# Kernel tuning notes

Measured on AMD Instinct MI355X. Metric: run time of the kernel, lower is better.

The kernel has to match this reference:

```python
import jax, jax.numpy as jnp
import numpy as np

NEG_SLOPE = 0.2


def _gat_layer(x, W, a_src, a_dst, b, src, dst, n_nodes, heads, dim):
    # x: [N, F_in]; W: [F_in, heads*dim]
    h = (x @ W).reshape(n_nodes, heads, dim)            # [N,H,D]
    e_src = (h * a_src).sum(-1)                          # [N,H]
    e_dst = (h * a_dst).sum(-1)                          # [N,H]
    e = jax.nn.leaky_relu(e_src[src] + e_dst[dst], NEG_SLOPE)  # [E,H]
    # edge softmax over incoming edges of each target node
    m = jax.ops.segment_max(e, dst, num_segments=n_nodes)      # [N,H]
    ex = jnp.exp(e - m[dst])
    denom = jax.ops.segment_sum(ex, dst, num_segments=n_nodes)  # [N,H]
    alpha = ex / denom[dst]                              # [E,H]
    out = jax.ops.segment_sum(h[src] * alpha[:, :, None], dst,
                              num_segments=n_nodes)      # [N,H,D]
    return out.reshape(n_nodes, heads * dim) + b


def setup_inputs() -> dict:
    key = jax.random.key(0)
    ks = jax.random.split(key, 10)
    N, E, F_in = 100000, 1600000, 300
    x = jax.random.normal(ks[0], (N, F_in), dtype=jnp.float32)
    edge_index = jax.random.randint(ks[1], (2, E), 0, N, dtype=jnp.int64)
    s = 0.1
    return {
        'x': x,
        'edge_index': edge_index,
        'W1': jax.random.normal(ks[2], (F_in, 64), jnp.float32) * s,
        'att_src1': jax.random.normal(ks[3], (8, 8), jnp.float32) * s,
        'att_dst1': jax.random.normal(ks[4], (8, 8), jnp.float32) * s,
        'b1': jax.random.normal(ks[5], (64,), jnp.float32) * s,
        'W2': jax.random.normal(ks[6], (64, 64), jnp.float32) * s,
        'att_src2': jax.random.normal(ks[7], (1, 64), jnp.float32) * s,
        'att_dst2': jax.random.normal(ks[8], (1, 64), jnp.float32) * s,
        'b2': jax.random.normal(ks[9], (64,), jnp.float32) * s,
    }


def reference(x, edge_index, W1, att_src1, att_dst1, b1, W2, att_src2, att_dst2, b2):
    N = x.shape[0]
    # add self-loops (PyG GATConv default)
    loop = jnp.arange(N, dtype=edge_index.dtype)
    src = jnp.concatenate([edge_index[0], loop])
    dst = jnp.concatenate([edge_index[1], loop])
    # dropout p=0.6 is identity in eval mode
    h = _gat_layer(x, W1, att_src1, att_dst1, b1, src, dst, N, 8, 8)    # [N,64]
    h = jax.nn.elu(h)
    h = _gat_layer(h, W2, att_src2, att_dst2, b2, src, dst, N, 1, 64)   # [N,64]
    return jax.nn.log_softmax(h, axis=1)
```

## Files before the change

### kernel.cpp

```cpp
#include <hip/hip_runtime.h>
#include <math.h>

using short8  = __attribute__((ext_vector_type(8))) short;
using ushort8 = __attribute__((ext_vector_type(8))) unsigned short;
using f32x4   = __attribute__((ext_vector_type(4))) float;

#define NBLKS 512
#define BPAD  800
#define EB 4

__device__ __forceinline__ unsigned short f2bf(float f) {
    unsigned u = __float_as_uint(f);
    unsigned r = u + 0x7FFF + ((u >> 16) & 1);
    return (unsigned short)(r >> 16);
}
__device__ __forceinline__ float bf2f(unsigned short v) {
    return __uint_as_float((unsigned)v << 16);
}
__device__ __forceinline__ unsigned cvt2(float lo, float hi) {
    unsigned r;
    asm("v_cvt_pk_bf16_f32 %0, %1, %2" : "=v"(r) : "v"(lo), "v"(hi));
    return r;
}


__global__ void detect64_kernel(const int* __restrict__ ei, int E, int* __restrict__ flag) {
    __shared__ int any;
    if (threadIdx.x == 0) any = 0;
    __syncthreads();
    for (int i = threadIdx.x; i < 1024; i += 256) {
        if (ei[2 * i + 1] != 0) { any = 1; break; }
    }
    __syncthreads();
    if (threadIdx.x == 0) *flag = (any ? 0 : 1);
}


__global__ __launch_bounds__(256) void binA_kernel(
    const int* __restrict__ ei, int E, int N, const int* __restrict__ flag,
    int nbuck, int* __restrict__ hist, int chunk) {
    __shared__ int lh[BPAD];
    for (int i = threadIdx.x; i < nbuck; i += 256) lh[i] = 0;
    __syncthreads();
    int is64 = *flag;
    int Etot = E + N;
    int beg = blockIdx.x * chunk, end = min(Etot, beg + chunk);
    for (int i = beg + threadIdx.x; i < end; i += 256) {
        int d = (i < E) ? (is64 ? ei[2 * (E + i)] : ei[E + i]) : (i - E);
        atomicAdd(&lh[d >> 7], 1);
    }
    __syncthreads();
    for (int i = threadIdx.x; i < nbuck; i += 256) hist[blockIdx.x * BPAD + i] = lh[i];
}

__global__ void scanBlocks_kernel(int* __restrict__ hist, int nbuck, int* __restrict__ bucketTotal) {
    int bin = blockIdx.x * 256 + threadIdx.x;
    if (bin >= nbuck) return;
    int run = 0;
    for (int b = 0; b < NBLKS; b++) {
        int v = hist[b * BPAD + bin];
        hist[b * BPAD + bin] = run;
        run += v;
    }
    bucketTotal[bin] = run;
}

__global__ void scanBucket_kernel(const int* __restrict__ bucketTotal, int nbuck,
                                  int* __restrict__ bucketBase) {
    __shared__ int s[1024];
    int t = threadIdx.x;
    int v = (t < nbuck) ? bucketTotal[t] : 0;
    s[t] = v;
    __syncthreads();
    for (int off = 1; off < 1024; off <<= 1) {
        int x = (t >= off) ? s[t - off] : 0;
        __syncthreads();
        s[t] += x;
        __syncthreads();
    }
    if (t < nbuck) bucketBase[t] = s[t] - v;
    if (t == nbuck - 1) bucketBase[nbuck] = s[t];
}

__global__ __launch_bounds__(256) void binB_kernel(
    const int* __restrict__ ei, int E, int N, const int* __restrict__ flag,
    int nbuck, const int* __restrict__ hist, const int* __restrict__ bucketBase,
    int* __restrict__ tmp, int chunk) {
    __shared__ int cur[BPAD];
    for (int i = threadIdx.x; i < nbuck; i += 256)
        cur[i] = bucketBase[i] + hist[blockIdx.x * BPAD + i];
    __syncthreads();
    int is64 = *flag;
    int Etot = E + N;
    int beg = blockIdx.x * chunk, end = min(Etot, beg + chunk);
    for (int i = beg + threadIdx.x; i < end; i += 256) {
        int s, d;
        if (i < E) {
            if (is64) { s = ei[2 * i]; d = ei[2 * (E + i)]; }
            else      { s = ei[i];     d = ei[E + i]; }
        } else { s = i - E; d = i - E; }
        int pos = atomicAdd(&cur[d >> 7], 1);
        tmp[pos] = ((d & 127) << 17) | s;
    }
}

__global__ __launch_bounds__(256) void binC_kernel(
    const int* __restrict__ tmp, const int* __restrict__ bucketBase, int nbuck,
    int N, int Etot, int* __restrict__ rowptr, int* __restrict__ col) {
    __shared__ int lh[128];
    __shared__ int cur[128];
    int g = blockIdx.x;
    int t = threadIdx.x;
    int beg = bucketBase[g], end = bucketBase[g + 1];
    if (t < 128) lh[t] = 0;
    __syncthreads();
    for (int i = beg + t; i < end; i += 256) atomicAdd(&lh[tmp[i] >> 17], 1);
    __syncthreads();
    int c = (t < 128) ? lh[t] : 0;
    for (int off = 1; off < 128; off <<= 1) {
        int x = 0;
        if (t < 128 && t >= off) x = lh[t - off];
        __syncthreads();
        if (t < 128) lh[t] += x;
        __syncthreads();
    }
    if (t < 128) {
        int excl = lh[t] - c;
        cur[t] = beg + excl;
        int node = g * 128 + t;
        if (node < N) rowptr[node] = beg + excl;
    }
    if (g == 0 && t == 0) rowptr[N] = Etot;
    if (g == 0 && t < 16) col[Etot + t] = 0;
    __syncthreads();
    for (int i = beg + t; i < end; i += 256) {
        int v = tmp[i];
        int pos = atomicAdd(&cur[v >> 17], 1);
        col[pos] = v & 0x1FFFF;
    }
}


__global__ __launch_bounds__(256) void gemm1_mfma_kernel(
    const float* __restrict__ x, const float* __restrict__ W,
    const float* __restrict__ asrc, const float* __restrict__ adst,
    unsigned short* __restrict__ hbf, float* __restrict__ es, float* __restrict__ ed, int N) {
    __shared__ __align__(16) unsigned short A_lds[128 * 40];
    __shared__ __align__(16) unsigned short B_lds[64 * 40];
    const int tx = threadIdx.x;
    const int wv = tx >> 6;
    const int lane = tx & 63;
    const int l15 = lane & 15;
    const int quad = lane >> 4;
    const int rowBase = blockIdx.x * 128;

    f32x4 acc[2][4];
#pragma unroll
    for (int rt = 0; rt < 2; rt++)
#pragma unroll
        for (int ct = 0; ct < 4; ct++) acc[rt][ct] = (f32x4){0.f, 0.f, 0.f, 0.f};

    const int kq = tx & 7;
    const int r0 = tx >> 3;
    const int colB = tx & 63;
    const int kkb = (tx >> 6) * 8;

    for (int k0 = 0; k0 < 320; k0 += 32) {
        bool kvalid = (k0 + kq * 4 + 4 <= 300);
#pragma unroll
        for (int p = 0; p < 4; p++) {
            int row = p * 32 + r0;
            int grow = rowBase + row;
            float4 v = make_float4(0.f, 0.f, 0.f, 0.f);
            if (kvalid && grow < N) v = *(const float4*)&x[(size_t)grow * 300 + k0 + kq * 4];
            *(uint2*)&A_lds[row * 40 + kq * 4] = make_uint2(cvt2(v.x, v.y), cvt2(v.z, v.w));
        }
        {
            float v0, v1, v2, v3, v4, v5, v6, v7;
            v0 = (k0 + kkb + 0 < 300) ? W[(size_t)(k0 + kkb + 0) * 64 + colB] : 0.f;
            v1 = (k0 + kkb + 1 < 300) ? W[(size_t)(k0 + kkb + 1) * 64 + colB] : 0.f;
            v2 = (k0 + kkb + 2 < 300) ? W[(size_t)(k0 + kkb + 2) * 64 + colB] : 0.f;
            v3 = (k0 + kkb + 3 < 300) ? W[(size_t)(k0 + kkb + 3) * 64 + colB] : 0.f;
            v4 = (k0 + kkb + 4 < 300) ? W[(size_t)(k0 + kkb + 4) * 64 + colB] : 0.f;
            v5 = (k0 + kkb + 5 < 300) ? W[(size_t)(k0 + kkb + 5) * 64 + colB] : 0.f;
            v6 = (k0 + kkb + 6 < 300) ? W[(size_t)(k0 + kkb + 6) * 64 + colB] : 0.f;
            v7 = (k0 + kkb + 7 < 300) ? W[(size_t)(k0 + kkb + 7) * 64 + colB] : 0.f;
            *(uint2*)&B_lds[colB * 40 + kkb]     = make_uint2(cvt2(v0, v1), cvt2(v2, v3));
            *(uint2*)&B_lds[colB * 40 + kkb + 4] = make_uint2(cvt2(v4, v5), cvt2(v6, v7));
        }
        __syncthreads();
        short8 af[2], bfr[4];
#pragma unroll
        for (int rt = 0; rt < 2; rt++)
            af[rt] = *(const short8*)&A_lds[(wv * 32 + rt * 16 + l15) * 40 + quad * 8];
#pragma unroll
        for (int ct = 0; ct < 4; ct++)
            bfr[ct] = *(const short8*)&B_lds[(ct * 16 + l15) * 40 + quad * 8];
#pragma unroll
        for (int rt = 0; rt < 2; rt++)
#pragma unroll
            for (int ct = 0; ct < 4; ct++)
                acc[rt][ct] = __builtin_amdgcn_mfma_f32_16x16x32_bf16(af[rt], bfr[ct], acc[rt][ct], 0, 0, 0);
        __syncthreads();
    }

    float as_v[4], ad_v[4];
#pragma unroll
    for (int ct = 0; ct < 4; ct++) {
        as_v[ct] = asrc[ct * 16 + l15];
        ad_v[ct] = adst[ct * 16 + l15];
    }
#pragma unroll
    for (int rt = 0; rt < 2; rt++) {
#pragma unroll
        for (int reg = 0; reg < 4; reg++) {
            int row = rowBase + wv * 32 + rt * 16 + quad * 4 + reg;
            bool ok = (row < N);
#pragma unroll
            for (int ct = 0; ct < 4; ct++) {
                float v = acc[rt][ct][reg];
                if (ok) hbf[(size_t)row * 64 + ct * 16 + l15] = f2bf(v);
                float ps = v * as_v[ct];
                float pd = v * ad_v[ct];
                ps += __shfl_xor(ps, 1); ps += __shfl_xor(ps, 2); ps += __shfl_xor(ps, 4);
                pd += __shfl_xor(pd, 1); pd += __shfl_xor(pd, 2); pd += __shfl_xor(pd, 4);
                if ((lane & 7) == 0 && ok) {
                    int head = 2 * ct + ((lane >> 3) & 1);
                    es[row * 8 + head] = ps;
                    ed[row * 8 + head] = pd;
                }
            }
        }
    }
}


__global__ __launch_bounds__(256) void gemm2_mfma_kernel(
    const unsigned short* __restrict__ xin, const float* __restrict__ W,
    const float* __restrict__ asrc, const float* __restrict__ adst,
    unsigned short* __restrict__ hbf, float* __restrict__ es, float* __restrict__ ed, int N) {
    __shared__ __align__(16) unsigned short A_lds[128 * 72];
    __shared__ __align__(16) unsigned short B_lds[64 * 72];
    const int tx = threadIdx.x;
    const int wv = tx >> 6;
    const int lane = tx & 63;
    const int l15 = lane & 15;
    const int quad = lane >> 4;
    const int rowBase = blockIdx.x * 128;

    f32x4 acc[2][4];
#pragma unroll
    for (int rt = 0; rt < 2; rt++)
#pragma unroll
        for (int ct = 0; ct < 4; ct++) acc[rt][ct] = (f32x4){0.f, 0.f, 0.f, 0.f};

    {
        int colB = tx & 63;
        int kk = (tx >> 6) * 16;
#pragma unroll
        for (int j = 0; j < 16; j++)
            B_lds[colB * 72 + kk + j] = f2bf(W[(size_t)(kk + j) * 64 + colB]);
    }
    {
        int kq = tx & 7, r0 = tx >> 3;
        const ushort8 z = (ushort8){0, 0, 0, 0, 0, 0, 0, 0};
#pragma unroll
        for (int p = 0; p < 4; p++) {
            int row = p * 32 + r0;
            int grow = rowBase + row;
            ushort8 v = z;
            if (grow < N) v = *(const ushort8*)&xin[(size_t)grow * 64 + kq * 8];
            *(ushort8*)&A_lds[row * 72 + kq * 8] = v;
        }
    }
    __syncthreads();
#pragma unroll
    for (int c = 0; c < 2; c++) {
        short8 af[2], bfr[4];
#pragma unroll
        for (int rt = 0; rt < 2; rt++)
            af[rt] = *(const short8*)&A_lds[(wv * 32 + rt * 16 + l15) * 72 + quad * 8 + c * 32];
#pragma unroll
        for (int ct = 0; ct < 4; ct++)
            bfr[ct] = *(const short8*)&B_lds[(ct * 16 + l15) * 72 + quad * 8 + c * 32];
#pragma unroll
        for (int rt = 0; rt < 2; rt++)
#pragma unroll
            for (int ct = 0; ct < 4; ct++)
                acc[rt][ct] = __builtin_amdgcn_mfma_f32_16x16x32_bf16(af[rt], bfr[ct], acc[rt][ct], 0, 0, 0);
    }

    float as_v[4], ad_v[4];
#pragma unroll
    for (int ct = 0; ct < 4; ct++) {
        as_v[ct] = asrc[ct * 16 + l15];
        ad_v[ct] = adst[ct * 16 + l15];
    }
#pragma unroll
    for (int rt = 0; rt < 2; rt++) {
#pragma unroll
        for (int reg = 0; reg < 4; reg++) {
            int row = rowBase + wv * 32 + rt * 16 + quad * 4 + reg;
            bool ok = (row < N);
            float ps = 0.f, pd = 0.f;
#pragma unroll
            for (int ct = 0; ct < 4; ct++) {
                float v = acc[rt][ct][reg];
                if (ok) hbf[(size_t)row * 64 + ct * 16 + l15] = f2bf(v);
                ps = fmaf(v, as_v[ct], ps);
                pd = fmaf(v, ad_v[ct], pd);
            }
            ps += __shfl_xor(ps, 1); ps += __shfl_xor(ps, 2);
            ps += __shfl_xor(ps, 4); ps += __shfl_xor(ps, 8);
            pd += __shfl_xor(pd, 1); pd += __shfl_xor(pd, 2);
            pd += __shfl_xor(pd, 4); pd += __shfl_xor(pd, 8);
            if (l15 == 0 && ok) { es[row] = ps; ed[row] = pd; }
        }
    }
}


__global__ __launch_bounds__(256) void agg1f_kernel(
    const int* __restrict__ rowptr, const int* __restrict__ col,
    const unsigned short* __restrict__ hbf, const float* __restrict__ es,
    const float* __restrict__ ed, const float* __restrict__ b,
    unsigned int* __restrict__ outbf, int N) {
    int node = blockIdx.x * 4 + (threadIdx.x >> 6);
    int lane = threadIdx.x & 63;
    if (node >= N) return;
    int half = lane >> 5, fl = lane & 31;
    int f0 = fl * 2, hh = fl >> 2;
    int beg = rowptr[node], end = rowptr[node + 1];
    float edv = ed[node * 8 + hh];
    float acc0 = 0.f, acc1 = 0.f, lsum = 0.f;
    for (int i = beg; i < end; i += 8) {
        int ei_[EB], ss[EB];
        float ev[EB];
        unsigned hp[EB];
#pragma unroll
        for (int j = 0; j < EB; j++) ei_[j] = i + 2 * j + half;
#pragma unroll
        for (int j = 0; j < EB; j++) ss[j] = col[(ei_[j] < end) ? ei_[j] : beg];
#pragma unroll
        for (int j = 0; j < EB; j++) ev[j] = es[ss[j] * 8 + hh];
#pragma unroll
        for (int j = 0; j < EB; j++) hp[j] = *(const unsigned*)&hbf[(size_t)ss[j] * 64 + f0];
#pragma unroll
        for (int j = 0; j < EB; j++) {
            float e = ev[j] + edv;
            e = (e > 0.f) ? e : 0.2f * e;
            float wj = __expf(fminf(e, 30.f));
            wj = (ei_[j] < end) ? wj : 0.f;
            lsum += wj;
            float lo = __uint_as_float(hp[j] << 16);
            float hi = __uint_as_float(hp[j] & 0xFFFF0000u);
            acc0 = fmaf(wj, lo, acc0);
            acc1 = fmaf(wj, hi, acc1);
        }
    }
    acc0 += __shfl_xor(acc0, 32);
    acc1 += __shfl_xor(acc1, 32);
    lsum += __shfl_xor(lsum, 32);
    float rinv = 1.f / lsum;
    float o0 = acc0 * rinv + b[f0];
    float o1 = acc1 * rinv + b[f0 + 1];
    o0 = (o0 > 0.f) ? o0 : expm1f(o0);
    o1 = (o1 > 0.f) ? o1 : expm1f(o1);
    if (half == 0) {
        unsigned pk = (unsigned)f2bf(o0) | ((unsigned)f2bf(o1) << 16);
        outbf[((size_t)node * 64 + f0) >> 1] = pk;
    }
}

__global__ __launch_bounds__(256) void agg2f_kernel(
    const int* __restrict__ rowptr, const int* __restrict__ col,
    const unsigned short* __restrict__ hbf, const float* __restrict__ es,
    const float* __restrict__ ed, const float* __restrict__ b,
    float* __restrict__ out, int N) {
    int node = blockIdx.x * 4 + (threadIdx.x >> 6);
    int lane = threadIdx.x & 63;
    if (node >= N) return;
    int half = lane >> 5, fl = lane & 31;
    int f0 = fl * 2;
    int beg = rowptr[node], end = rowptr[node + 1];
    float edv = ed[node];
    float acc0 = 0.f, acc1 = 0.f, lsum = 0.f;
    for (int i = beg; i < end; i += 8) {
        int ei_[EB], ss[EB];
        float ev[EB];
        unsigned hp[EB];
#pragma unroll
        for (int j = 0; j < EB; j++) ei_[j] = i + 2 * j + half;
#pragma unroll
        for (int j = 0; j < EB; j++) ss[j] = col[(ei_[j] < end) ? ei_[j] : beg];
#pragma unroll
        for (int j = 0; j < EB; j++) ev[j] = es[ss[j]];
#pragma unroll
        for (int j = 0; j < EB; j++) hp[j] = *(const unsigned*)&hbf[(size_t)ss[j] * 64 + f0];
#pragma unroll
        for (int j = 0; j < EB; j++) {
            float e = ev[j] + edv;
            e = (e > 0.f) ? e : 0.2f * e;
            float wj = __expf(fminf(e, 30.f));
            wj = (ei_[j] < end) ? wj : 0.f;
            lsum += wj;
            float lo = __uint_as_float(hp[j] << 16);
            float hi = __uint_as_float(hp[j] & 0xFFFF0000u);
            acc0 = fmaf(wj, lo, acc0);
            acc1 = fmaf(wj, hi, acc1);
        }
    }
    acc0 += __shfl_xor(acc0, 32);
    acc1 += __shfl_xor(acc1, 32);
    lsum += __shfl_xor(lsum, 32);
    float rinv = 1.f / lsum;
    float o0 = acc0 * rinv + b[f0];
    float o1 = acc1 * rinv + b[f0 + 1];
    float M = fmaxf(o0, o1);
    M = fmaxf(M, __shfl_xor(M, 1));  M = fmaxf(M, __shfl_xor(M, 2));
    M = fmaxf(M, __shfl_xor(M, 4));  M = fmaxf(M, __shfl_xor(M, 8));
    M = fmaxf(M, __shfl_xor(M, 16));
    float se = __expf(o0 - M) + __expf(o1 - M);
    se += __shfl_xor(se, 1);  se += __shfl_xor(se, 2);
    se += __shfl_xor(se, 4);  se += __shfl_xor(se, 8);
    se += __shfl_xor(se, 16);
    float ls = logf(se);
    if (half == 0) {
        float2 r = make_float2(o0 - M - ls, o1 - M - ls);
        *(float2*)&out[(size_t)node * 64 + f0] = r;
    }
}


extern "C" void kernel_launch(void* const* d_in, const int* in_sizes, int n_in,
                              void* d_out, int out_size, void* d_ws, size_t ws_size,
                              hipStream_t stream) {
    const float* x   = (const float*)d_in[0];
    const int*   ei  = (const int*)d_in[1];
    const float* W1  = (const float*)d_in[2];
    const float* as1 = (const float*)d_in[3];
    const float* ad1 = (const float*)d_in[4];
    const float* b1  = (const float*)d_in[5];
    const float* W2  = (const float*)d_in[6];
    const float* as2 = (const float*)d_in[7];
    const float* ad2 = (const float*)d_in[8];
    const float* b2  = (const float*)d_in[9];
    const int N = in_sizes[0] / 300;
    const int E = in_sizes[1] / 2;
    const int Etot = E + N;
    const int nbuck = (N + 127) >> 7;
    (void)n_in; (void)out_size; (void)ws_size;

    char* w = (char*)d_ws;
    auto alloc = [&](size_t bytes) -> char* {
        char* p = w;
        w += (bytes + 255) & ~(size_t)255;
        return p;
    };
    int*   flag        = (int*)alloc(256);
    int*   hist        = (int*)alloc((size_t)NBLKS * BPAD * 4);
    int*   bucketTotal = (int*)alloc((size_t)(BPAD + 1) * 4);
    int*   bucketBase  = (int*)alloc((size_t)(BPAD + 1) * 4);
    int*   tmp         = (int*)alloc((size_t)(Etot + 16) * 4);
    int*   rowptr      = (int*)alloc((size_t)(N + 1) * 4);
    int*   col         = (int*)alloc((size_t)(Etot + 16) * 4);
    unsigned short* h1  = (unsigned short*)alloc((size_t)N * 64 * 2);
    unsigned short* h1p = (unsigned short*)alloc((size_t)N * 64 * 2);
    float* es1         = (float*)alloc((size_t)N * 8 * 4);
    float* ed1         = (float*)alloc((size_t)N * 8 * 4);
    float* es2         = (float*)alloc((size_t)N * 4);
    float* ed2         = (float*)alloc((size_t)N * 4);
    unsigned short* h2 = h1;

    detect64_kernel<<<1, 256, 0, stream>>>(ei, E, flag);

    int chunk = (Etot + NBLKS - 1) / NBLKS;
    binA_kernel<<<NBLKS, 256, 0, stream>>>(ei, E, N, flag, nbuck, hist, chunk);
    scanBlocks_kernel<<<(nbuck + 255) / 256, 256, 0, stream>>>(hist, nbuck, bucketTotal);
    scanBucket_kernel<<<1, 1024, 0, stream>>>(bucketTotal, nbuck, bucketBase);
    binB_kernel<<<NBLKS, 256, 0, stream>>>(ei, E, N, flag, nbuck, hist, bucketBase, tmp, chunk);
    binC_kernel<<<nbuck, 256, 0, stream>>>(tmp, bucketBase, nbuck, N, Etot, rowptr, col);

    gemm1_mfma_kernel<<<(N + 127) / 128, 256, 0, stream>>>(x, W1, as1, ad1, h1, es1, ed1, N);
    agg1f_kernel<<<(N + 3) / 4, 256, 0, stream>>>(rowptr, col, h1, es1, ed1, b1,
                                                  (unsigned int*)h1p, N);
    gemm2_mfma_kernel<<<(N + 127) / 128, 256, 0, stream>>>(h1p, W2, as2, ad2, h2, es2, ed2, N);
    agg2f_kernel<<<(N + 3) / 4, 256, 0, stream>>>(rowptr, col, h2, es2, ed2, b2, (float*)d_out, N);
}
```

Baseline: 438.0 us.

## Interleave source attention scores into padded feature rows and batch-load neighbor indices

After: 432.0 us. Within noise of the previous version (-1.4%).

```diff
diff --git a/kernel.cpp b/kernel.cpp
--- a/kernel.cpp
+++ b/kernel.cpp
@@ -8,6 +8,7 @@
 #define NBLKS 512
 #define BPAD  800
 #define EB 4
+#define HSTR 80
 
 __device__ __forceinline__ unsigned short f2bf(float f) {
     unsigned u = __float_as_uint(f);
@@ -131,7 +132,7 @@
         if (node < N) rowptr[node] = beg + excl;
     }
     if (g == 0 && t == 0) rowptr[N] = Etot;
-    if (g == 0 && t < 16) col[Etot + t] = 0;
+    if (g == 0 && t < 64) col[Etot + t] = 0;
     __syncthreads();
     for (int i = beg + t; i < end; i += 256) {
         int v = tmp[i];
@@ -144,7 +145,7 @@
 __global__ __launch_bounds__(256) void gemm1_mfma_kernel(
     const float* __restrict__ x, const float* __restrict__ W,
     const float* __restrict__ asrc, const float* __restrict__ adst,
-    unsigned short* __restrict__ hbf, float* __restrict__ es, float* __restrict__ ed, int N) {
+    unsigned short* __restrict__ hbf, float* __restrict__ ed, int N) {
     __shared__ __align__(16) unsigned short A_lds[128 * 40];
     __shared__ __align__(16) unsigned short B_lds[64 * 40];
     const int tx = threadIdx.x;
@@ -219,14 +220,14 @@
 #pragma unroll
             for (int ct = 0; ct < 4; ct++) {
                 float v = acc[rt][ct][reg];
-                if (ok) hbf[(size_t)row * 64 + ct * 16 + l15] = f2bf(v);
+                if (ok) hbf[(size_t)row * HSTR + ct * 16 + l15] = f2bf(v);
                 float ps = v * as_v[ct];
                 float pd = v * ad_v[ct];
                 ps += __shfl_xor(ps, 1); ps += __shfl_xor(ps, 2); ps += __shfl_xor(ps, 4);
                 pd += __shfl_xor(pd, 1); pd += __shfl_xor(pd, 2); pd += __shfl_xor(pd, 4);
                 if ((lane & 7) == 0 && ok) {
                     int head = 2 * ct + ((lane >> 3) & 1);
-                    es[row * 8 + head] = ps;
+                    *(float*)((char*)hbf + (size_t)row * (HSTR * 2) + 128 + 4 * head) = ps;
                     ed[row * 8 + head] = pd;
                 }
             }
@@ -238,7 +239,7 @@
 __global__ __launch_bounds__(256) void gemm2_mfma_kernel(
     const unsigned short* __restrict__ xin, const float* __restrict__ W,
     const float* __restrict__ asrc, const float* __restrict__ adst,
-    unsigned short* __restrict__ hbf, float* __restrict__ es, float* __restrict__ ed, int N) {
+    unsigned short* __restrict__ hbf, float* __restrict__ ed, int N) {
     __shared__ __align__(16) unsigned short A_lds[128 * 72];
     __shared__ __align__(16) unsigned short B_lds[64 * 72];
     const int tx = threadIdx.x;
@@ -306,7 +307,7 @@
 #pragma unroll
             for (int ct = 0; ct < 4; ct++) {
                 float v = acc[rt][ct][reg];
-                if (ok) hbf[(size_t)row * 64 + ct * 16 + l15] = f2bf(v);
+                if (ok) hbf[(size_t)row * HSTR + ct * 16 + l15] = f2bf(v);
                 ps = fmaf(v, as_v[ct], ps);
                 pd = fmaf(v, ad_v[ct], pd);
             }
@@ -314,7 +315,10 @@
             ps += __shfl_xor(ps, 4); ps += __shfl_xor(ps, 8);
             pd += __shfl_xor(pd, 1); pd += __shfl_xor(pd, 2);
             pd += __shfl_xor(pd, 4); pd += __shfl_xor(pd, 8);
-            if (l15 == 0 && ok) { es[row] = ps; ed[row] = pd; }
+            if (l15 == 0 && ok) {
+                *(float*)((char*)hbf + (size_t)row * (HSTR * 2) + 128) = ps;
+                ed[row] = pd;
+            }
         }
     }
 }
@@ -322,9 +326,8 @@
 
 __global__ __launch_bounds__(256) void agg1f_kernel(
     const int* __restrict__ rowptr, const int* __restrict__ col,
-    const unsigned short* __restrict__ hbf, const float* __restrict__ es,
-    const float* __restrict__ ed, const float* __restrict__ b,
-    unsigned int* __restrict__ outbf, int N) {
+    const unsigned short* __restrict__ hbf, const float* __restrict__ ed,
+    const float* __restrict__ b, unsigned int* __restrict__ outbf, int N) {
     int node = blockIdx.x * 4 + (threadIdx.x >> 6);
     int lane = threadIdx.x & 63;
     if (node >= N) return;
@@ -332,30 +335,40 @@
     int f0 = fl * 2, hh = fl >> 2;
     int beg = rowptr[node], end = rowptr[node + 1];
     float edv = ed[node * 8 + hh];
+    const char* hb = (const char*)hbf;
     float acc0 = 0.f, acc1 = 0.f, lsum = 0.f;
-    for (int i = beg; i < end; i += 8) {
-        int ei_[EB], ss[EB];
-        float ev[EB];
-        unsigned hp[EB];
-#pragma unroll
-        for (int j = 0; j < EB; j++) ei_[j] = i + 2 * j + half;
-#pragma unroll
-        for (int j = 0; j < EB; j++) ss[j] = col[(ei_[j] < end) ? ei_[j] : beg];
-#pragma unroll
-        for (int j = 0; j < EB; j++) ev[j] = es[ss[j] * 8 + hh];
-#pragma unroll
-        for (int j = 0; j < EB; j++) hp[j] = *(const unsigned*)&hbf[(size_t)ss[j] * 64 + f0];
-#pragma unroll
-        for (int j = 0; j < EB; j++) {
-            float e = ev[j] + edv;
-            e = (e > 0.f) ? e : 0.2f * e;
-            float wj = __expf(fminf(e, 30.f));
-            wj = (ei_[j] < end) ? wj : 0.f;
-            lsum += wj;
-            float lo = __uint_as_float(hp[j] << 16);
-            float hi = __uint_as_float(hp[j] & 0xFFFF0000u);
-            acc0 = fmaf(wj, lo, acc0);
-            acc1 = fmaf(wj, hi, acc1);
+    for (int i0 = beg; i0 < end; i0 += 64) {
+        int idx = i0 + lane;
+        int cv = col[idx < end ? idx : beg];
+        int lim = min(64, end - i0);
+        for (int s = 0; s < lim; s += 8) {
+            int ss[EB], vld[EB];
+            float ev[EB];
+            unsigned hp[EB];
+#pragma unroll
+            for (int j = 0; j < EB; j++) {
+                int sl = s + 2 * j + half;
+                ss[j] = __shfl(cv, sl);
+                vld[j] = (i0 + sl < end);
+            }
+#pragma unroll
+            for (int j = 0; j < EB; j++)
+                ev[j] = *(const float*)(hb + (size_t)ss[j] * (HSTR * 2) + 128 + 4 * hh);
+#pragma unroll
+            for (int j = 0; j < EB; j++)
+                hp[j] = *(const unsigned*)(hb + (size_t)ss[j] * (HSTR * 2) + 4 * fl);
+#pragma unroll
+            for (int j = 0; j < EB; j++) {
+                float e = ev[j] + edv;
+                e = (e > 0.f) ? e : 0.2f * e;
+                float wj = __expf(fminf(e, 30.f));
+                wj = vld[j] ? wj : 0.f;
+                lsum += wj;
+                float lo = __uint_as_float(hp[j] << 16);
+                float hi = __uint_as_float(hp[j] & 0xFFFF0000u);
+                acc0 = fmaf(wj, lo, acc0);
+                acc1 = fmaf(wj, hi, acc1);
+            }
         }
     }
     acc0 += __shfl_xor(acc0, 32);
@@ -374,9 +387,8 @@
 
 __global__ __launch_bounds__(256) void agg2f_kernel(
     const int* __restrict__ rowptr, const int* __restrict__ col,
-    const unsigned short* __restrict__ hbf, const float* __restrict__ es,
-    const float* __restrict__ ed, const float* __restrict__ b,
-    float* __restrict__ out, int N) {
+    const unsigned short* __restrict__ hbf, const float* __restrict__ ed,
+    const float* __restrict__ b, float* __restrict__ out, int N) {
     int node = blockIdx.x * 4 + (threadIdx.x >> 6);
     int lane = threadIdx.x & 63;
     if (node >= N) return;
@@ -384,30 +396,40 @@
     int f0 = fl * 2;
     int beg = rowptr[node], end = rowptr[node + 1];
     float edv = ed[node];
+    const char* hb = (const char*)hbf;
     float acc0 = 0.f, acc1 = 0.f, lsum = 0.f;
-    for (int i = beg; i < end; i += 8) {
-        int ei_[EB], ss[EB];
-        float ev[EB];
-        unsigned hp[EB];
-#pragma unroll
-        for (int j = 0; j < EB; j++) ei_[j] = i + 2 * j + half;
-#pragma unroll
-        for (int j = 0; j < EB; j++) ss[j] = col[(ei_[j] < end) ? ei_[j] : beg];
-#pragma unroll
-        for (int j = 0; j < EB; j++) ev[j] = es[ss[j]];
-#pragma unroll
-        for (int j = 0; j < EB; j++) hp[j] = *(const unsigned*)&hbf[(size_t)ss[j] * 64 + f0];
-#pragma unroll
-        for (int j = 0; j < EB; j++) {
-            float e = ev[j] + edv;
-            e = (e > 0.f) ? e : 0.2f * e;
-            float wj = __expf(fminf(e, 30.f));
-            wj = (ei_[j] < end) ? wj : 0.f;
-            lsum += wj;
-            float lo = __uint_as_float(hp[j] << 16);
-            float hi = __uint_as_float(hp[j] & 0xFFFF0000u);
-            acc0 = fmaf(wj, lo, acc0);
-            acc1 = fmaf(wj, hi, acc1);
+    for (int i0 = beg; i0 < end; i0 += 64) {
+        int idx = i0 + lane;
+        int cv = col[idx < end ? idx : beg];
+        int lim = min(64, end - i0);
+        for (int s = 0; s < lim; s += 8) {
+            int ss[EB], vld[EB];
+            float ev[EB];
+            unsigned hp[EB];
+#pragma unroll
+            for (int j = 0; j < EB; j++) {
+                int sl = s + 2 * j + half;
+                ss[j] = __shfl(cv, sl);
+                vld[j] = (i0 + sl < end);
+            }
+#pragma unroll
+            for (int j = 0; j < EB; j++)
+                ev[j] = *(const float*)(hb + (size_t)ss[j] * (HSTR * 2) + 128);
+#pragma unroll
+            for (int j = 0; j < EB; j++)
+                hp[j] = *(const unsigned*)(hb + (size_t)ss[j] * (HSTR * 2) + 4 * fl);
+#pragma unroll
+            for (int j = 0; j < EB; j++) {
+                float e = ev[j] + edv;
+                e = (e > 0.f) ? e : 0.2f * e;
+                float wj = __expf(fminf(e, 30.f));
+                wj = vld[j] ? wj : 0.f;
+                lsum += wj;
+                float lo = __uint_as_float(hp[j] << 16);
+                float hi = __uint_as_float(hp[j] & 0xFFFF0000u);
+                acc0 = fmaf(wj, lo, acc0);
+                acc1 = fmaf(wj, hi, acc1);
+            }
         }
     }
     acc0 += __shfl_xor(acc0, 32);
@@ -461,16 +483,14 @@
     int*   hist        = (int*)alloc((size_t)NBLKS * BPAD * 4);
     int*   bucketTotal = (int*)alloc((size_t)(BPAD + 1) * 4);
     int*   bucketBase  = (int*)alloc((size_t)(BPAD + 1) * 4);
-    int*   tmp         = (int*)alloc((size_t)(Etot + 16) * 4);
+    int*   tmp         = (int*)alloc((size_t)(Etot + 64) * 4);
     int*   rowptr      = (int*)alloc((size_t)(N + 1) * 4);
-    int*   col         = (int*)alloc((size_t)(Etot + 16) * 4);
-    unsigned short* h1  = (unsigned short*)alloc((size_t)N * 64 * 2);
+    int*   col         = (int*)alloc((size_t)(Etot + 64) * 4);
+    unsigned short* h1x = (unsigned short*)alloc((size_t)N * HSTR * 2);
     unsigned short* h1p = (unsigned short*)alloc((size_t)N * 64 * 2);
-    float* es1         = (float*)alloc((size_t)N * 8 * 4);
     float* ed1         = (float*)alloc((size_t)N * 8 * 4);
-    float* es2         = (float*)alloc((size_t)N * 4);
     float* ed2         = (float*)alloc((size_t)N * 4);
-    unsigned short* h2 = h1;
+    unsigned short* h2x = h1x;
 
     detect64_kernel<<<1, 256, 0, stream>>>(ei, E, flag);
 
@@ -481,9 +501,9 @@
     binB_kernel<<<NBLKS, 256, 0, stream>>>(ei, E, N, flag, nbuck, hist, bucketBase, tmp, chunk);
     binC_kernel<<<nbuck, 256, 0, stream>>>(tmp, bucketBase, nbuck, N, Etot, rowptr, col);
 
-    gemm1_mfma_kernel<<<(N + 127) / 128, 256, 0, stream>>>(x, W1, as1, ad1, h1, es1, ed1, N);
-    agg1f_kernel<<<(N + 3) / 4, 256, 0, stream>>>(rowptr, col, h1, es1, ed1, b1,
+    gemm1_mfma_kernel<<<(N + 127) / 128, 256, 0, stream>>>(x, W1, as1, ad1, h1x, ed1, N);
+    agg1f_kernel<<<(N + 3) / 4, 256, 0, stream>>>(rowptr, col, h1x, ed1, b1,
                                                   (unsigned int*)h1p, N);
-    gemm2_mfma_kernel<<<(N + 127) / 128, 256, 0, stream>>>(h1p, W2, as2, ad2, h2, es2, ed2, N);
-    agg2f_kernel<<<(N + 3) / 4, 256, 0, stream>>>(rowptr, col, h2, es2, ed2, b2, (float*)d_out, N);
-}
+    gemm2_mfma_kernel<<<(N + 127) / 128, 256, 0, stream>>>(h1p, W2, as2, ad2, h2x, ed2, N);
+    agg2f_kernel<<<(N + 3) / 4, 256, 0, stream>>>(rowptr, col, h2x, ed2, b2, (float*)d_out, N);
+}
```
